# Kernel optimization log

Hardware: AMD Instinct MI355X
Metric: run time of the kernel (lower is better)

## Reference

```python
import jax, jax.numpy as jnp
from jax import lax
import numpy as np

G = 33            # LUT grid size per axis (hard-coded in module)
G3 = G * G * G    # 35937 entries per channel LUT


def _gelu(x):
    return jax.nn.gelu(x, approximate=False)  # torch nn.GELU default = exact erf


def _conv(x, w, b):
    # 3x3 stride-1 padding-1 conv == SAME padding, NCHW/OIHW like torch
    y = lax.conv_general_dilated(x, w, (1, 1), 'SAME',
                                 dimension_numbers=('NCHW', 'OIHW', 'NCHW'))
    return y + b[None, :, None, None]


def _bn(x, g, b, eps=1e-5):
    # eval-mode BatchNorm2d with running_mean=0, running_var=1
    s = g * (1.0 + eps) ** -0.5
    return x * s[None, :, None, None] + b[None, :, None, None]


def _resblock(x, wA, bA, gA, btA, wB, bB, gB, btB):
    h = _gelu(_bn(_conv(x, wA, bA), gA, btA))
    h = _bn(_conv(h, wB, bB), gB, btB)
    return _gelu(h + x)


def _apply_luts(luts_flat, recon):
    # Trilinear 3D-LUT sampling == F.grid_sample(mode='bilinear', padding_mode='border',
    # align_corners=True) on a 5D LUT. grid = recon[...,[2,1,0]]*2-1 means image ch0 (R)
    # indexes LUT dim 2, ch1 (G) dim 3, ch2 (B) dim 4; align_corners maps v->v*(G-1).
    # luts_flat: [B, L*3, G^3] (all num_luts fused into the channel dim, gathered once)
    # recon:     [B, 3, H, W] in [0,1]
    B, C3, _ = luts_flat.shape
    _, _, H, W = recon.shape
    c = jnp.clip(recon * (G - 1.0), 0.0, G - 1.0)      # border clamp
    f0 = jnp.clip(jnp.floor(c), 0.0, G - 2.0)
    t = c - f0                                          # fractional weights [B,3,H,W]
    i0 = f0.astype(jnp.int32)
    r0, g0, b0 = i0[:, 0], i0[:, 1], i0[:, 2]           # [B,H,W] each
    tr, tg, tb = t[:, 0], t[:, 1], t[:, 2]
    out = jnp.zeros((B, C3, H * W), dtype=luts_flat.dtype)
    for dr in (0, 1):
        for dg in (0, 1):
            for db in (0, 1):
                idx = ((r0 + dr) * G + (g0 + dg)) * G + (b0 + db)   # [B,H,W]
                w = ((tr if dr else 1.0 - tr) * (tg if dg else 1.0 - tg)
                     * (tb if db else 1.0 - tb))
                vals = jnp.take_along_axis(luts_flat, idx.reshape(B, 1, H * W), axis=2)
                out = out + vals * w.reshape(B, 1, H * W)
    return out.reshape(B, C3 // 3, 3, H, W)            # [B, L, 3, H, W]


def setup_inputs() -> dict:
    key = jax.random.key(0)
    ks = iter(jax.random.split(key, 32))
    def nrm(shape, s=0.02):
        return jax.random.normal(next(ks), shape, jnp.float32) * s
    B, T, V, E, HID, L, H, W = 4, 1024, 1024, 256, 256, 8, 384, 384
    inp = dict(
        tokens=jax.random.randint(next(ks), (B, T), 0, V),
        img=jax.random.uniform(next(ks), (B, 3, H, W), jnp.float32),
        recon_image=jax.random.uniform(next(ks), (B, 3, H, W), jnp.float32),
        emb_table=nrm((V, E)),
        agg_w1=nrm((E, HID)), agg_b1=jnp.zeros((HID,), jnp.float32),
        agg_w2=nrm((HID, HID)), agg_b2=jnp.zeros((HID,), jnp.float32),
        lut_w1=nrm((HID, HID)), lut_b1=jnp.zeros((HID,), jnp.float32),
        lut_w2=nrm((HID, L * 3 * G3), 0.005),
        lut_b2=jnp.zeros((L * 3 * G3,), jnp.float32),
        wg_w1=nrm((HID, HID // 4)), wg_b1=jnp.zeros((HID // 4,), jnp.float32),
        wg_w2=nrm((HID // 4, L)), wg_b2=jnp.zeros((L,), jnp.float32),
        rp_cin_w=nrm((32, 3, 3, 3)), rp_cin_b=jnp.zeros((32,), jnp.float32),
        rp_rbA_w=nrm((32, 32, 3, 3)), rp_rbA_b=jnp.zeros((32,), jnp.float32),
        rp_rbA_g=jnp.ones((32,), jnp.float32), rp_rbA_bt=jnp.zeros((32,), jnp.float32),
        rp_rbB_w=nrm((32, 32, 3, 3)), rp_rbB_b=jnp.zeros((32,), jnp.float32),
        rp_rbB_g=jnp.ones((32,), jnp.float32), rp_rbB_bt=jnp.zeros((32,), jnp.float32),
        rp_cout_w=nrm((3, 32, 3, 3)), rp_cout_b=jnp.zeros((3,), jnp.float32),
        fu_cin_w=nrm((32, 6, 3, 3)), fu_cin_b=jnp.zeros((32,), jnp.float32),
        fu_rbA_w=nrm((32, 32, 3, 3)), fu_rbA_b=jnp.zeros((32,), jnp.float32),
        fu_rbA_g=jnp.ones((32,), jnp.float32), fu_rbA_bt=jnp.zeros((32,), jnp.float32),
        fu_rbB_w=nrm((32, 32, 3, 3)), fu_rbB_b=jnp.zeros((32,), jnp.float32),
        fu_rbB_g=jnp.ones((32,), jnp.float32), fu_rbB_bt=jnp.zeros((32,), jnp.float32),
        fu_cout_w=nrm((3, 32, 3, 3)), fu_cout_b=jnp.zeros((3,), jnp.float32),
    )
    return inp


def reference(tokens, img, recon_image, emb_table,
              agg_w1, agg_b1, agg_w2, agg_b2,
              lut_w1, lut_b1, lut_w2, lut_b2,
              wg_w1, wg_b1, wg_w2, wg_b2,
              rp_cin_w, rp_cin_b, rp_rbA_w, rp_rbA_b, rp_rbA_g, rp_rbA_bt,
              rp_rbB_w, rp_rbB_b, rp_rbB_g, rp_rbB_bt, rp_cout_w, rp_cout_b,
              fu_cin_w, fu_cin_b, fu_rbA_w, fu_rbA_b, fu_rbA_g, fu_rbA_bt,
              fu_rbB_w, fu_rbB_b, fu_rbB_g, fu_rbB_bt, fu_cout_w, fu_cout_b):
    B = img.shape[0]
    L = wg_w2.shape[1]
    # token features
    emb = emb_table[tokens]                       # [B, T, E]
    tf = jnp.mean(emb, axis=1)                    # [B, E]
    tf = _gelu(tf @ agg_w1 + agg_b1) @ agg_w2 + agg_b2   # [B, HID]
    # dynamic LUTs and fusion weights
    lut_params = _gelu(tf @ lut_w1 + lut_b1) @ lut_w2 + lut_b2   # [B, L*3*G3]
    luts_flat = lut_params.reshape(B, L * 3, G3)
    lw = jax.nn.softmax(_gelu(tf @ wg_w1 + wg_b1) @ wg_w2 + wg_b2, axis=1)  # [B, L]
    # apply all LUTs in one fused gather pass, then weighted sum over LUTs
    lut_out = _apply_luts(luts_flat, recon_image)                # [B, L, 3, H, W]
    fused = jnp.einsum('blchw,bl->bchw', lut_out, lw)            # [B, 3, H, W]
    # residual processing branch on original img
    proc = _gelu(_conv(img, rp_cin_w, rp_cin_b))
    proc = _resblock(proc, rp_rbA_w, rp_rbA_b, rp_rbA_g, rp_rbA_bt,
                     rp_rbB_w, rp_rbB_b, rp_rbB_g, rp_rbB_bt)
    proc = _conv(proc, rp_cout_w, rp_cout_b)
    # fusion
    comb = jnp.concatenate([fused, proc], axis=1)                # [B, 6, H, W]
    out = _gelu(_conv(comb, fu_cin_w, fu_cin_b))
    out = _resblock(out, fu_rbA_w, fu_rbA_b, fu_rbA_g, fu_rbA_bt,
                    fu_rbB_w, fu_rbB_b, fu_rbB_g, fu_rbB_bt)
    out = _conv(out, fu_cout_w, fu_cout_b)
    return out + img
```

## Files before the change

kernel.cpp:

```cpp
#include <hip/hip_runtime.h>
#include <hip/hip_bf16.h>
#include <math.h>

#define BB    4
#define TT    1024
#define EE    256
#define HIDD  256
#define LLUT  8
#define HGT   384
#define WID   384
#define HWPX  147456
#define GSZ   33
#define G3    35937
#define NCOL  862488

typedef __attribute__((ext_vector_type(8))) short bf16x8;
typedef __attribute__((ext_vector_type(4))) float f32x4;

__device__ __forceinline__ float gelu_f(float x) {
    float s = 1.5957691216057308f * x * (1.0f + 0.044715f * x * x);
    float e = __expf(s);
    return x - x / (e + 1.0f);
}

__device__ __forceinline__ ushort f2bf(float x) {
    uint u = __float_as_uint(x);
    return (ushort)((u + 0x7FFFu + ((u >> 16) & 1u)) >> 16);
}
__device__ __forceinline__ uint pack2bf(float a, float b) {
    return (uint)f2bf(a) | ((uint)f2bf(b) << 16);
}
__device__ __forceinline__ float bf2f_lo(uint u) { return __uint_as_float(u << 16); }
__device__ __forceinline__ float bf2f_hi(uint u) { return __uint_as_float(u & 0xFFFF0000u); }

__global__ __launch_bounds__(256) void pack_wconv_kernel(
    const float* __restrict__ w0, const float* __restrict__ w1,
    const float* __restrict__ w2, const float* __restrict__ w3,
    ushort* __restrict__ wpk)
{
    const int layer = blockIdx.x;
    const float* w = (layer == 0) ? w0 : (layer == 1) ? w1 : (layer == 2) ? w2 : w3;
    ushort* dst = wpk + layer * 9216;
    for (int i = threadIdx.x; i < 9216; i += 256) {
        const int j    = i & 7;
        const int lane = (i >> 3) & 63;
        const int half = (i >> 9) & 1;
        const int tap  = i >> 10;
        const int co = half * 16 + (lane & 15);
        const int ci = (lane >> 4) * 8 + j;
        dst[i] = f2bf(w[co * 288 + ci * 9 + tap]);
    }
}

__global__ __launch_bounds__(256) void emb_partial_kernel(
    const int* __restrict__ tokens, const float* __restrict__ emb,
    float* __restrict__ partial)
{
    const int s = blockIdx.x, b = blockIdx.y, tid = threadIdx.x;
    const int* tok = tokens + b * TT + s * 16;
    float acc = 0.f;
#pragma unroll
    for (int t = 0; t < 16; ++t) acc += emb[tok[t] * EE + tid];
    partial[(b * 64 + s) * EE + tid] = acc;
}

__global__ __launch_bounds__(1024) void mlp_head_kernel(
    const float* __restrict__ partial,
    const float* __restrict__ aw1, const float* __restrict__ ab1,
    const float* __restrict__ aw2, const float* __restrict__ ab2,
    const float* __restrict__ lw1, const float* __restrict__ lb1,
    const float* __restrict__ gw1, const float* __restrict__ gb1,
    const float* __restrict__ gw2, const float* __restrict__ gb2,
    float* __restrict__ h3_out, float* __restrict__ lw_out)
{
    const int b = blockIdx.x;
    const int tid = threadIdx.x;
    const int o = tid & 255;
    const int q = tid >> 8;
    __shared__ float tf[256], h1[256], tf2s[256], h4[64], lg[8];
    __shared__ float red[4][256];

    {
        float acc = 0.f;
#pragma unroll
        for (int s = 0; s < 16; ++s)
            acc += partial[(b * 64 + q * 16 + s) * EE + o];
        red[q][o] = acc;
    }
    __syncthreads();
    if (tid < 256)
        tf[tid] = (red[0][tid] + red[1][tid] + red[2][tid] + red[3][tid]) * (1.0f / TT);
    __syncthreads();

    {
        float s = 0.f;
#pragma unroll 8
        for (int j = 0; j < 64; ++j) {
            const int k = (q << 6) + j;
            s += tf[k] * aw1[k * HIDD + o];
        }
        red[q][o] = s;
    }
    __syncthreads();
    if (tid < 256)
        h1[tid] = gelu_f(red[0][tid] + red[1][tid] + red[2][tid] + red[3][tid] + ab1[tid]);
    __syncthreads();

    {
        float s = 0.f;
#pragma unroll 8
        for (int j = 0; j < 64; ++j) {
            const int k = (q << 6) + j;
            s += h1[k] * aw2[k * HIDD + o];
        }
        red[q][o] = s;
    }
    __syncthreads();
    if (tid < 256)
        tf2s[tid] = red[0][tid] + red[1][tid] + red[2][tid] + red[3][tid] + ab2[tid];
    __syncthreads();

    {
        float s = 0.f;
#pragma unroll 8
        for (int j = 0; j < 64; ++j) {
            const int k = (q << 6) + j;
            s += tf2s[k] * lw1[k * HIDD + o];
        }
        red[q][o] = s;
    }
    __syncthreads();
    if (tid < 256)
        h3_out[b * HIDD + tid] =
            gelu_f(red[0][tid] + red[1][tid] + red[2][tid] + red[3][tid] + lb1[tid]);
    __syncthreads();

    {
        const int o64 = tid & 63, q16 = tid >> 6;
        float s = 0.f;
#pragma unroll
        for (int j = 0; j < 16; ++j) {
            const int k = q16 * 16 + j;
            s += tf2s[k] * gw1[k * 64 + o64];
        }
        ((float*)red)[q16 * 64 + o64] = s;
    }
    __syncthreads();
    if (tid < 64) {
        float s = gb1[tid];
#pragma unroll
        for (int r = 0; r < 16; ++r) s += ((float*)red)[r * 64 + tid];
        h4[tid] = gelu_f(s);
    }
    __syncthreads();

    if (tid < 8) {
        float s = gb2[tid];
#pragma unroll 8
        for (int k = 0; k < 64; ++k) s += h4[k] * gw2[k * LLUT + tid];
        lg[tid] = s;
    }
    __syncthreads();
    if (tid == 0) {
        float m = lg[0];
        for (int i = 1; i < LLUT; ++i) m = fmaxf(m, lg[i]);
        float ssum = 0.f, ex[LLUT];
        for (int i = 0; i < LLUT; ++i) { ex[i] = expf(lg[i] - m); ssum += ex[i]; }
        for (int i = 0; i < LLUT; ++i) lw_out[b * LLUT + i] = ex[i] / ssum;
    }
}

__global__ __launch_bounds__(256) void lut_fused_kernel(
    const float* __restrict__ h3, const float* __restrict__ lwv,
    const float* __restrict__ w2, const float* __restrict__ b2,
    float* __restrict__ clut)
{
    __shared__ float h[BB * HIDD];
    __shared__ float lws[BB * LLUT];
    const int tid = threadIdx.x;
    for (int i = tid; i < BB * HIDD; i += 256) h[i] = h3[i];
    if (tid < BB * LLUT) lws[tid] = lwv[tid];
    __syncthreads();

    const int idx = blockIdx.x * 256 + tid;
    if (idx >= 3 * G3) return;
    const int c = idx / G3, v = idx - c * G3;

    float acc[BB][LLUT];
#pragma unroll
    for (int b = 0; b < BB; ++b)
#pragma unroll
        for (int l = 0; l < LLUT; ++l) acc[b][l] = 0.f;

    const float* wbase = w2 + (long)c * G3 + v;
#pragma unroll 4
    for (int k = 0; k < HIDD; ++k) {
        const float* row = wbase + (long)k * NCOL;
        float wl[LLUT];
#pragma unroll
        for (int l = 0; l < LLUT; ++l) wl[l] = row[l * 3 * G3];
#pragma unroll
        for (int b = 0; b < BB; ++b) {
            const float hb = h[b * HIDD + k];
#pragma unroll
            for (int l = 0; l < LLUT; ++l) acc[b][l] += wl[l] * hb;
        }
    }

    float bb[LLUT];
#pragma unroll
    for (int l = 0; l < LLUT; ++l) bb[l] = b2[(long)(l * 3 + c) * G3 + v];

#pragma unroll
    for (int b = 0; b < BB; ++b) {
        float s = 0.f;
#pragma unroll
        for (int l = 0; l < LLUT; ++l) s += lws[b * LLUT + l] * (acc[b][l] + bb[l]);
        clut[(long)(b * 3 + c) * G3 + v] = s;
    }
}

__global__ __launch_bounds__(256) void applylut_out3_kernel(
    const float* __restrict__ clut, const float* __restrict__ recon,
    const ushort* __restrict__ act2, const float* __restrict__ wgt,
    const float* __restrict__ bias, ushort* __restrict__ comb)
{
    const int p = blockIdx.x * 256 + threadIdx.x;
    const int b = blockIdx.y;

    const float* rc = recon + (long)b * 3 * HWPX;
    float cr = fminf(fmaxf(rc[p] * 32.f, 0.f), 32.f);
    float cg = fminf(fmaxf(rc[HWPX + p] * 32.f, 0.f), 32.f);
    float cb = fminf(fmaxf(rc[2 * HWPX + p] * 32.f, 0.f), 32.f);
    float fr = fminf(floorf(cr), 31.f);
    float fg = fminf(floorf(cg), 31.f);
    float fb = fminf(floorf(cb), 31.f);
    float tr = cr - fr, tg = cg - fg, tb_ = cb - fb;
    int idx = (((int)fr * GSZ + (int)fg) * GSZ + (int)fb);
    float c[3];
#pragma unroll
    for (int ch = 0; ch < 3; ++ch) {
        const float* lut = clut + (long)(b * 3 + ch) * G3;
        float v000 = lut[idx],                  v001 = lut[idx + 1];
        float v010 = lut[idx + GSZ],            v011 = lut[idx + GSZ + 1];
        float v100 = lut[idx + GSZ * GSZ],      v101 = lut[idx + GSZ * GSZ + 1];
        float v110 = lut[idx + GSZ * GSZ + GSZ], v111 = lut[idx + GSZ * GSZ + GSZ + 1];
        float c00 = v000 + (v001 - v000) * tb_;
        float c01 = v010 + (v011 - v010) * tb_;
        float c10 = v100 + (v101 - v100) * tb_;
        float c11 = v110 + (v111 - v110) * tb_;
        float c0 = c00 + (c01 - c00) * tg;
        float c1 = c10 + (c11 - c10) * tg;
        c[ch] = c0 + (c1 - c0) * tr;
    }

    const int hh = p / WID, ww = p - hh * WID;
    float acc[3] = {bias[0], bias[1], bias[2]};
#pragma unroll
    for (int tap = 0; tap < 9; ++tap) {
        const int dh = tap / 3, dw = tap - dh * 3;
        const int gh = hh + dh - 1, gw = ww + dw - 1;
        if (gh < 0 || gh >= HGT || gw < 0 || gw >= WID) continue;
        const uint4* xp = (const uint4*)(act2 + ((long)b * HWPX + gh * WID + gw) * 32);
        float xx[32];
#pragma unroll
        for (int q = 0; q < 4; ++q) {
            uint4 v = xp[q];
            xx[q * 8 + 0] = bf2f_lo(v.x); xx[q * 8 + 1] = bf2f_hi(v.x);
            xx[q * 8 + 2] = bf2f_lo(v.y); xx[q * 8 + 3] = bf2f_hi(v.y);
            xx[q * 8 + 4] = bf2f_lo(v.z); xx[q * 8 + 5] = bf2f_hi(v.z);
            xx[q * 8 + 6] = bf2f_lo(v.w); xx[q * 8 + 7] = bf2f_hi(v.w);
        }
#pragma unroll
        for (int o = 0; o < 3; ++o)
#pragma unroll
            for (int ci = 0; ci < 32; ++ci)
                acc[o] += xx[ci] * wgt[o * 288 + ci * 9 + tap];
    }

    uint4 u;
    u.x = pack2bf(c[0], c[1]);
    u.y = pack2bf(c[2], 0.f);
    u.z = pack2bf(acc[0], acc[1]);
    u.w = pack2bf(acc[2], 0.f);
    *(uint4*)(comb + ((long)b * HWPX + p) * 8) = u;
}

__global__ __launch_bounds__(256) void conv_in3_kernel(
    const float* __restrict__ img, const float* __restrict__ wgt,
    const float* __restrict__ bias, ushort* __restrict__ out)
{
    const int tid = threadIdx.x;
    const int p0 = (blockIdx.x * 256 + tid) * 2;
    const int b = blockIdx.y;
    const int hh = p0 / WID, ww = p0 - hh * WID;

    float acc[32][2];
#pragma unroll
    for (int o = 0; o < 32; ++o) { float bv = bias[o]; acc[o][0] = bv; acc[o][1] = bv; }

    const bool wlo = (ww > 0), whi = (ww + 2 < WID);
#pragma unroll
    for (int ci = 0; ci < 3; ++ci) {
        const float* ip = img + (long)(b * 3 + ci) * HWPX;
        float x[3][4];
#pragma unroll
        for (int dh = 0; dh < 3; ++dh) {
            const int hs = hh + dh - 1;
            const bool hok = (hs >= 0) && (hs < HGT);
            const float* rp_ = ip + hs * WID + ww;
            x[dh][0] = (hok && wlo) ? rp_[-1] : 0.f;
            x[dh][1] = hok ? rp_[0] : 0.f;
            x[dh][2] = hok ? rp_[1] : 0.f;
            x[dh][3] = (hok && whi) ? rp_[2] : 0.f;
        }
#pragma unroll
        for (int o = 0; o < 32; ++o) {
            const float* wv = wgt + o * 27 + ci * 9;
#pragma unroll
            for (int dh = 0; dh < 3; ++dh)
#pragma unroll
                for (int dw = 0; dw < 3; ++dw) {
                    const float w = wv[dh * 3 + dw];
                    acc[o][0] += x[dh][dw]     * w;
                    acc[o][1] += x[dh][dw + 1] * w;
                }
        }
    }

    ushort* op = out + ((long)b * HWPX + p0) * 32;
#pragma unroll
    for (int px = 0; px < 2; ++px) {
        uint u[16];
#pragma unroll
        for (int o2 = 0; o2 < 16; ++o2)
            u[o2] = pack2bf(gelu_f(acc[2 * o2][px]), gelu_f(acc[2 * o2 + 1][px]));
        uint4* dst = (uint4*)(op + px * 32);
#pragma unroll
        for (int q = 0; q < 4; ++q)
            dst[q] = make_uint4(u[4 * q], u[4 * q + 1], u[4 * q + 2], u[4 * q + 3]);
    }
}

#define TH2 8
#define TW2 64
#define NTX (WID / TW2)
#define NTY (HGT / TH2)
#define NBLK (NTX * NTY * BB)
#define CHUNK (NBLK / 8)
#define HALO_H2 10
#define HALO_W2 66
#define CSTR 40

template <bool HAS_RES>
__global__ __launch_bounds__(512, 6) void conv32_mfma(
    const ushort* __restrict__ in, const ushort* __restrict__ res,
    const ushort* __restrict__ wpk, const float* __restrict__ bias,
    const float* __restrict__ bn_g, const float* __restrict__ bn_bt,
    ushort* __restrict__ out)
{
    __shared__ ushort halo[HALO_H2 * HALO_W2 * CSTR];
    __shared__ float s_scale[32], s_shift[32];

    const int tid = threadIdx.x;
    const int bid = blockIdx.x;
    const int t   = (bid & 7) * CHUNK + (bid >> 3);
    const int tx  = t % NTX;
    const int rem = t / NTX;
    const int ty  = rem % NTY;
    const int b   = rem / NTY;
    const int h0 = ty * TH2;
    const int w0 = tx * TW2;

    if (tid < 32) {
        float sg = bn_g[tid] * 0.9999950000375f;
        s_scale[tid] = sg;
        s_shift[tid] = bias[tid] * sg + bn_bt[tid];
    }

    const ushort* inb = in + (long)b * HWPX * 32;
    for (int i = tid; i < HALO_H2 * HALO_W2 * 4; i += 512) {
        const int row = i / (HALO_W2 * 4);
        const int rem2 = i - row * (HALO_W2 * 4);
        const int px = rem2 >> 2, q = rem2 & 3;
        const int gh = h0 + row - 1, gw = w0 + px - 1;
        uint4 v = make_uint4(0u, 0u, 0u, 0u);
        if (gh >= 0 && gh < HGT && gw >= 0 && gw < WID)
            v = *(const uint4*)(inb + ((long)gh * WID + gw) * 32 + q * 8);
        *(uint4*)(&halo[(row * HALO_W2 + px) * CSTR + q * 8]) = v;
    }
    __syncthreads();

    const int lane = tid & 63, wid = tid >> 6;
    const int l15 = lane & 15, kg = lane >> 4;
    const int r = wid;
    const ushort* wlane = wpk + lane * 8;

    f32x4 acc[4][2];
#pragma unroll
    for (int f = 0; f < 4; ++f)
#pragma unroll
        for (int cf = 0; cf < 2; ++cf)
            acc[f][cf] = (f32x4){0.f, 0.f, 0.f, 0.f};

#pragma unroll
    for (int tap = 0; tap < 9; ++tap) {
        const int dh = tap / 3, dw = tap - dh * 3;
        const bf16x8 a0 = *(const bf16x8*)(wlane + (tap * 2 + 0) * 512);
        const bf16x8 a1 = *(const bf16x8*)(wlane + (tap * 2 + 1) * 512);
#pragma unroll
        for (int f = 0; f < 4; ++f) {
            const int c0 = f * 16;
            const bf16x8 bfv = *(const bf16x8*)(
                &halo[((r + dh) * HALO_W2 + (c0 + dw + l15)) * CSTR + kg * 8]);
            acc[f][0] = __builtin_amdgcn_mfma_f32_16x16x32_bf16(a0, bfv, acc[f][0], 0, 0, 0);
            acc[f][1] = __builtin_amdgcn_mfma_f32_16x16x32_bf16(a1, bfv, acc[f][1], 0, 0, 0);
        }
    }

#pragma unroll
    for (int f = 0; f < 4; ++f) {
        const int c0 = f * 16;
        const long gpx = (long)b * HWPX + (long)(h0 + r) * WID + (w0 + c0 + l15);
#pragma unroll
        for (int cf = 0; cf < 2; ++cf) {
            const int co0 = cf * 16 + kg * 4;
            const float4 sc = *(const float4*)(&s_scale[co0]);
            const float4 sh = *(const float4*)(&s_shift[co0]);
            float v0 = acc[f][cf][0] * sc.x + sh.x;
            float v1 = acc[f][cf][1] * sc.y + sh.y;
            float v2 = acc[f][cf][2] * sc.z + sh.z;
            float v3 = acc[f][cf][3] * sc.w + sh.w;
            if (HAS_RES) {
                const uint2 rv = *(const uint2*)(res + gpx * 32 + co0);
                v0 += bf2f_lo(rv.x); v1 += bf2f_hi(rv.x);
                v2 += bf2f_lo(rv.y); v3 += bf2f_hi(rv.y);
            }
            uint2 o;
            o.x = pack2bf(gelu_f(v0), gelu_f(v1));
            o.y = pack2bf(gelu_f(v2), gelu_f(v3));
            *(uint2*)(out + gpx * 32 + co0) = o;
        }
    }
}

__global__ __launch_bounds__(256) void conv_in6_kernel(
    const ushort* __restrict__ comb, const float* __restrict__ wgt,
    const float* __restrict__ bias, ushort* __restrict__ out)
{
    const int p = blockIdx.x * 256 + threadIdx.x;
    const int b = blockIdx.y;
    const int hh = p / WID, ww = p - hh * WID;

    float acc[32];
#pragma unroll
    for (int o = 0; o < 32; ++o) acc[o] = bias[o];

#pragma unroll
    for (int tap = 0; tap < 9; ++tap) {
        const int dh = tap / 3, dw = tap - dh * 3;
        const int gh = hh + dh - 1, gw = ww + dw - 1;
        if (gh < 0 || gh >= HGT || gw < 0 || gw >= WID) continue;
        const uint4 v = *(const uint4*)(comb + ((long)b * HWPX + gh * WID + gw) * 8);
        const float xs[6] = {bf2f_lo(v.x), bf2f_hi(v.x), bf2f_lo(v.y),
                             bf2f_lo(v.z), bf2f_hi(v.z), bf2f_lo(v.w)};
#pragma unroll
        for (int o = 0; o < 32; ++o) {
            const float* wv = wgt + o * 54 + tap;
            acc[o] += xs[0] * wv[0]  + xs[1] * wv[9]  + xs[2] * wv[18]
                    + xs[3] * wv[27] + xs[4] * wv[36] + xs[5] * wv[45];
        }
    }

    ushort* op = out + ((long)b * HWPX + p) * 32;
    uint u[16];
#pragma unroll
    for (int o2 = 0; o2 < 16; ++o2)
        u[o2] = pack2bf(gelu_f(acc[2 * o2]), gelu_f(acc[2 * o2 + 1]));
    uint4* dst = (uint4*)op;
#pragma unroll
    for (int q = 0; q < 4; ++q)
        dst[q] = make_uint4(u[4 * q], u[4 * q + 1], u[4 * q + 2], u[4 * q + 3]);
}

__global__ __launch_bounds__(256) void conv_final_kernel(
    const ushort* __restrict__ in, const float* __restrict__ wgt,
    const float* __restrict__ bias, const float* __restrict__ img,
    float* __restrict__ outp)
{
    const int p = blockIdx.x * 256 + threadIdx.x;
    const int b = blockIdx.y;
    const int hh = p / WID, ww = p - hh * WID;
    float acc[3] = {bias[0], bias[1], bias[2]};

#pragma unroll
    for (int tap = 0; tap < 9; ++tap) {
        const int dh = tap / 3, dw = tap - dh * 3;
        const int gh = hh + dh - 1, gw = ww + dw - 1;
        if (gh < 0 || gh >= HGT || gw < 0 || gw >= WID) continue;
        const uint4* xp = (const uint4*)(in + ((long)b * HWPX + gh * WID + gw) * 32);
        float xx[32];
#pragma unroll
        for (int q = 0; q < 4; ++q) {
            uint4 v = xp[q];
            xx[q * 8 + 0] = bf2f_lo(v.x); xx[q * 8 + 1] = bf2f_hi(v.x);
            xx[q * 8 + 2] = bf2f_lo(v.y); xx[q * 8 + 3] = bf2f_hi(v.y);
            xx[q * 8 + 4] = bf2f_lo(v.z); xx[q * 8 + 5] = bf2f_hi(v.z);
            xx[q * 8 + 6] = bf2f_lo(v.w); xx[q * 8 + 7] = bf2f_hi(v.w);
        }
#pragma unroll
        for (int o = 0; o < 3; ++o)
#pragma unroll
            for (int ci = 0; ci < 32; ++ci)
                acc[o] += xx[ci] * wgt[o * 288 + ci * 9 + tap];
    }
#pragma unroll
    for (int o = 0; o < 3; ++o)
        outp[(long)(b * 3 + o) * HWPX + p] = acc[o] + img[(long)(b * 3 + o) * HWPX + p];
}

extern "C" void kernel_launch(void* const* d_in, const int* in_sizes, int n_in,
                              void* d_out, int out_size, void* d_ws, size_t ws_size,
                              hipStream_t stream)
{
    const int*   tokens  = (const int*)d_in[0];
    const float* img     = (const float*)d_in[1];
    const float* recon   = (const float*)d_in[2];
    const float* emb     = (const float*)d_in[3];
    const float* agg_w1  = (const float*)d_in[4];
    const float* agg_b1  = (const float*)d_in[5];
    const float* agg_w2  = (const float*)d_in[6];
    const float* agg_b2  = (const float*)d_in[7];
    const float* lut_w1  = (const float*)d_in[8];
    const float* lut_b1  = (const float*)d_in[9];
    const float* lut_w2  = (const float*)d_in[10];
    const float* lut_b2  = (const float*)d_in[11];
    const float* wg_w1   = (const float*)d_in[12];
    const float* wg_b1   = (const float*)d_in[13];
    const float* wg_w2   = (const float*)d_in[14];
    const float* wg_b2   = (const float*)d_in[15];
    const float* rp_cin_w = (const float*)d_in[16];
    const float* rp_cin_b = (const float*)d_in[17];
    const float* rp_rbA_w = (const float*)d_in[18];
    const float* rp_rbA_b = (const float*)d_in[19];
    const float* rp_rbA_g = (const float*)d_in[20];
    const float* rp_rbA_bt= (const float*)d_in[21];
    const float* rp_rbB_w = (const float*)d_in[22];
    const float* rp_rbB_b = (const float*)d_in[23];
    const float* rp_rbB_g = (const float*)d_in[24];
    const float* rp_rbB_bt= (const float*)d_in[25];
    const float* rp_cout_w= (const float*)d_in[26];
    const float* rp_cout_b= (const float*)d_in[27];
    const float* fu_cin_w = (const float*)d_in[28];
    const float* fu_cin_b = (const float*)d_in[29];
    const float* fu_rbA_w = (const float*)d_in[30];
    const float* fu_rbA_b = (const float*)d_in[31];
    const float* fu_rbA_g = (const float*)d_in[32];
    const float* fu_rbA_bt= (const float*)d_in[33];
    const float* fu_rbB_w = (const float*)d_in[34];
    const float* fu_rbB_b = (const float*)d_in[35];
    const float* fu_rbB_g = (const float*)d_in[36];
    const float* fu_rbB_bt= (const float*)d_in[37];
    const float* fu_cout_w= (const float*)d_in[38];
    const float* fu_cout_b= (const float*)d_in[39];

    float* ws = (float*)d_ws;
    float*  h3      = ws;
    float*  lwv     = ws + 1024;
    float*  partial = ws + 2048;
    float*  clut    = ws + 69632;
    ushort* wpack   = (ushort*)(ws + 524288);
    ushort* comb    = (ushort*)(ws + 589824);
    ushort* act0    = (ushort*)(ws + 3145728);
    ushort* act1    = (ushort*)(ws + 12582912);
    ushort* act2    = (ushort*)(ws + 22020096);
    float*  outp    = (float*)d_out;

    pack_wconv_kernel<<<dim3(4), dim3(256), 0, stream>>>(
        rp_rbA_w, rp_rbB_w, fu_rbA_w, fu_rbB_w, wpack);

    emb_partial_kernel<<<dim3(64, BB), dim3(256), 0, stream>>>(tokens, emb, partial);
    mlp_head_kernel<<<dim3(BB), dim3(1024), 0, stream>>>(
        partial, agg_w1, agg_b1, agg_w2, agg_b2,
        lut_w1, lut_b1, wg_w1, wg_b1, wg_w2, wg_b2, h3, lwv);

    lut_fused_kernel<<<dim3((3 * G3 + 255) / 256), dim3(256), 0, stream>>>(
        h3, lwv, lut_w2, lut_b2, clut);

    const dim3 g1(HWPX / 256, BB), g2(HWPX / 512, BB), blk(256);
    const dim3 gm(NBLK), bm(512);

    conv_in3_kernel<<<g2, blk, 0, stream>>>(img, rp_cin_w, rp_cin_b, act0);
    conv32_mfma<false><<<gm, bm, 0, stream>>>(
        act0, nullptr, wpack + 0 * 9216, rp_rbA_b, rp_rbA_g, rp_rbA_bt, act1);
    conv32_mfma<true><<<gm, bm, 0, stream>>>(
        act1, act0, wpack + 1 * 9216, rp_rbB_b, rp_rbB_g, rp_rbB_bt, act2);

    applylut_out3_kernel<<<g1, blk, 0, stream>>>(
        clut, recon, act2, rp_cout_w, rp_cout_b, comb);

    conv_in6_kernel<<<g1, blk, 0, stream>>>(comb, fu_cin_w, fu_cin_b, act0);
    conv32_mfma<false><<<gm, bm, 0, stream>>>(
        act0, nullptr, wpack + 2 * 9216, fu_rbA_b, fu_rbA_g, fu_rbA_bt, act1);
    conv32_mfma<true><<<gm, bm, 0, stream>>>(
        act1, act0, wpack + 3 * 9216, fu_rbB_b, fu_rbB_g, fu_rbB_bt, act2);
    conv_final_kernel<<<g1, blk, 0, stream>>>(act2, fu_cout_w, fu_cout_b, img, outp);
}
```

Measured before the change: 553.0 us.

## Split LUT generation across the first three residual-branch conv launches

```diff
diff --git a/kernel.cpp b/kernel.cpp
--- a/kernel.cpp
+++ b/kernel.cpp
@@ -13,6 +13,7 @@
 #define GSZ   33
 #define G3    35937
 #define NCOL  862488
+#define NOUT3 107811
 
 typedef __attribute__((ext_vector_type(8))) short bf16x8;
 typedef __attribute__((ext_vector_type(4))) float f32x4;
@@ -32,6 +33,49 @@
 }
 __device__ __forceinline__ float bf2f_lo(uint u) { return __uint_as_float(u << 16); }
 __device__ __forceinline__ float bf2f_hi(uint u) { return __uint_as_float(u & 0xFFFF0000u); }
+
+__device__ __forceinline__ void lut_one(
+    int idx, const float* __restrict__ hbuf,
+    const float* __restrict__ w2, const float* __restrict__ b2,
+    float* __restrict__ clut)
+{
+    if (idx >= NOUT3) return;
+    const int c = idx / G3, v = idx - c * G3;
+    const float* lws = hbuf + BB * HIDD;
+
+    float acc[BB][LLUT];
+#pragma unroll
+    for (int b = 0; b < BB; ++b)
+#pragma unroll
+        for (int l = 0; l < LLUT; ++l) acc[b][l] = 0.f;
+
+    const float* wbase = w2 + (long)c * G3 + v;
+#pragma unroll 4
+    for (int k = 0; k < HIDD; ++k) {
+        const float* row = wbase + (long)k * NCOL;
+        float wl[LLUT];
+#pragma unroll
+        for (int l = 0; l < LLUT; ++l) wl[l] = row[l * 3 * G3];
+#pragma unroll
+        for (int b = 0; b < BB; ++b) {
+            const float hb = hbuf[b * HIDD + k];
+#pragma unroll
+            for (int l = 0; l < LLUT; ++l) acc[b][l] += wl[l] * hb;
+        }
+    }
+
+    float bb[LLUT];
+#pragma unroll
+    for (int l = 0; l < LLUT; ++l) bb[l] = b2[(long)(l * 3 + c) * G3 + v];
+
+#pragma unroll
+    for (int b = 0; b < BB; ++b) {
+        float s = 0.f;
+#pragma unroll
+        for (int l = 0; l < LLUT; ++l) s += lws[b * LLUT + l] * (acc[b][l] + bb[l]);
+        clut[(long)(b * 3 + c) * G3 + v] = s;
+    }
+}
 
 __global__ __launch_bounds__(256) void pack_wconv_kernel(
     const float* __restrict__ w0, const float* __restrict__ w1,
@@ -170,129 +214,31 @@
     }
 }
 
-__global__ __launch_bounds__(256) void lut_fused_kernel(
+#define IN3_NB   1152
+#define LUT1_NB  108
+#define LUT1_CNT 27648
+
+__global__ __launch_bounds__(256) void conv_in3_lut_kernel(
+    const float* __restrict__ img, const float* __restrict__ wgt,
+    const float* __restrict__ bias, ushort* __restrict__ out,
     const float* __restrict__ h3, const float* __restrict__ lwv,
     const float* __restrict__ w2, const float* __restrict__ b2,
     float* __restrict__ clut)
 {
-    __shared__ float h[BB * HIDD];
-    __shared__ float lws[BB * LLUT];
+    __shared__ float hbuf[BB * HIDD + BB * LLUT];
     const int tid = threadIdx.x;
-    for (int i = tid; i < BB * HIDD; i += 256) h[i] = h3[i];
-    if (tid < BB * LLUT) lws[tid] = lwv[tid];
-    __syncthreads();
-
-    const int idx = blockIdx.x * 256 + tid;
-    if (idx >= 3 * G3) return;
-    const int c = idx / G3, v = idx - c * G3;
-
-    float acc[BB][LLUT];
-#pragma unroll
-    for (int b = 0; b < BB; ++b)
-#pragma unroll
-        for (int l = 0; l < LLUT; ++l) acc[b][l] = 0.f;
-
-    const float* wbase = w2 + (long)c * G3 + v;
-#pragma unroll 4
-    for (int k = 0; k < HIDD; ++k) {
-        const float* row = wbase + (long)k * NCOL;
-        float wl[LLUT];
-#pragma unroll
-        for (int l = 0; l < LLUT; ++l) wl[l] = row[l * 3 * G3];
-#pragma unroll
-        for (int b = 0; b < BB; ++b) {
-            const float hb = h[b * HIDD + k];
-#pragma unroll
-            for (int l = 0; l < LLUT; ++l) acc[b][l] += wl[l] * hb;
-        }
-    }
-
-    float bb[LLUT];
-#pragma unroll
-    for (int l = 0; l < LLUT; ++l) bb[l] = b2[(long)(l * 3 + c) * G3 + v];
-
-#pragma unroll
-    for (int b = 0; b < BB; ++b) {
-        float s = 0.f;
-#pragma unroll
-        for (int l = 0; l < LLUT; ++l) s += lws[b * LLUT + l] * (acc[b][l] + bb[l]);
-        clut[(long)(b * 3 + c) * G3 + v] = s;
-    }
-}
-
-__global__ __launch_bounds__(256) void applylut_out3_kernel(
-    const float* __restrict__ clut, const float* __restrict__ recon,
-    const ushort* __restrict__ act2, const float* __restrict__ wgt,
-    const float* __restrict__ bias, ushort* __restrict__ comb)
-{
-    const int p = blockIdx.x * 256 + threadIdx.x;
-    const int b = blockIdx.y;
-
-    const float* rc = recon + (long)b * 3 * HWPX;
-    float cr = fminf(fmaxf(rc[p] * 32.f, 0.f), 32.f);
-    float cg = fminf(fmaxf(rc[HWPX + p] * 32.f, 0.f), 32.f);
-    float cb = fminf(fmaxf(rc[2 * HWPX + p] * 32.f, 0.f), 32.f);
-    float fr = fminf(floorf(cr), 31.f);
-    float fg = fminf(floorf(cg), 31.f);
-    float fb = fminf(floorf(cb), 31.f);
-    float tr = cr - fr, tg = cg - fg, tb_ = cb - fb;
-    int idx = (((int)fr * GSZ + (int)fg) * GSZ + (int)fb);
-    float c[3];
-#pragma unroll
-    for (int ch = 0; ch < 3; ++ch) {
-        const float* lut = clut + (long)(b * 3 + ch) * G3;
-        float v000 = lut[idx],                  v001 = lut[idx + 1];
-        float v010 = lut[idx + GSZ],            v011 = lut[idx + GSZ + 1];
-        float v100 = lut[idx + GSZ * GSZ],      v101 = lut[idx + GSZ * GSZ + 1];
-        float v110 = lut[idx + GSZ * GSZ + GSZ], v111 = lut[idx + GSZ * GSZ + GSZ + 1];
-        float c00 = v000 + (v001 - v000) * tb_;
-        float c01 = v010 + (v011 - v010) * tb_;
-        float c10 = v100 + (v101 - v100) * tb_;
-        float c11 = v110 + (v111 - v110) * tb_;
-        float c0 = c00 + (c01 - c00) * tg;
-        float c1 = c10 + (c11 - c10) * tg;
-        c[ch] = c0 + (c1 - c0) * tr;
-    }
-
-    const int hh = p / WID, ww = p - hh * WID;
-    float acc[3] = {bias[0], bias[1], bias[2]};
-#pragma unroll
-    for (int tap = 0; tap < 9; ++tap) {
-        const int dh = tap / 3, dw = tap - dh * 3;
-        const int gh = hh + dh - 1, gw = ww + dw - 1;
-        if (gh < 0 || gh >= HGT || gw < 0 || gw >= WID) continue;
-        const uint4* xp = (const uint4*)(act2 + ((long)b * HWPX + gh * WID + gw) * 32);
-        float xx[32];
-#pragma unroll
-        for (int q = 0; q < 4; ++q) {
-            uint4 v = xp[q];
-            xx[q * 8 + 0] = bf2f_lo(v.x); xx[q * 8 + 1] = bf2f_hi(v.x);
-            xx[q * 8 + 2] = bf2f_lo(v.y); xx[q * 8 + 3] = bf2f_hi(v.y);
-            xx[q * 8 + 4] = bf2f_lo(v.z); xx[q * 8 + 5] = bf2f_hi(v.z);
-            xx[q * 8 + 6] = bf2f_lo(v.w); xx[q * 8 + 7] = bf2f_hi(v.w);
-        }
-#pragma unroll
-        for (int o = 0; o < 3; ++o)
-#pragma unroll
-            for (int ci = 0; ci < 32; ++ci)
-                acc[o] += xx[ci] * wgt[o * 288 + ci * 9 + tap];
-    }
-
-    uint4 u;
-    u.x = pack2bf(c[0], c[1]);
-    u.y = pack2bf(c[2], 0.f);
-    u.z = pack2bf(acc[0], acc[1]);
-    u.w = pack2bf(acc[2], 0.f);
-    *(uint4*)(comb + ((long)b * HWPX + p) * 8) = u;
-}
-
-__global__ __launch_bounds__(256) void conv_in3_kernel(
-    const float* __restrict__ img, const float* __restrict__ wgt,
-    const float* __restrict__ bias, ushort* __restrict__ out)
-{
-    const int tid = threadIdx.x;
-    const int p0 = (blockIdx.x * 256 + tid) * 2;
-    const int b = blockIdx.y;
+    const int bid = blockIdx.x;
+
+    if (bid >= IN3_NB) {
+        for (int i = tid; i < BB * HIDD; i += 256) hbuf[i] = h3[i];
+        if (tid < BB * LLUT) hbuf[BB * HIDD + tid] = lwv[tid];
+        __syncthreads();
+        lut_one((bid - IN3_NB) * 256 + tid, hbuf, w2, b2, clut);
+        return;
+    }
+
+    const int b = bid / 288, xb = bid - b * 288;
+    const int p0 = (xb * 256 + tid) * 2;
     const int hh = p0 / WID, ww = p0 - hh * WID;
 
     float acc[32][2];
@@ -357,13 +303,26 @@
     const ushort* __restrict__ in, const ushort* __restrict__ res,
     const ushort* __restrict__ wpk, const float* __restrict__ bias,
     const float* __restrict__ bn_g, const float* __restrict__ bn_bt,
-    ushort* __restrict__ out)
+    ushort* __restrict__ out,
+    const float* __restrict__ h3, const float* __restrict__ lwv,
+    const float* __restrict__ w2, const float* __restrict__ b2,
+    float* __restrict__ clut, int lut_off)
 {
     __shared__ ushort halo[HALO_H2 * HALO_W2 * CSTR];
     __shared__ float s_scale[32], s_shift[32];
 
     const int tid = threadIdx.x;
     const int bid = blockIdx.x;
+
+    if (bid >= NBLK) {
+        float* hbuf = (float*)halo;
+        for (int i = tid; i < BB * HIDD; i += 512) hbuf[i] = h3[i];
+        if (tid < BB * LLUT) hbuf[BB * HIDD + tid] = lwv[tid];
+        __syncthreads();
+        lut_one((bid - NBLK) * 512 + tid + lut_off, hbuf, w2, b2, clut);
+        return;
+    }
+
     const int t   = (bid & 7) * CHUNK + (bid >> 3);
     const int tx  = t % NTX;
     const int rem = t / NTX;
@@ -442,6 +401,72 @@
             *(uint2*)(out + gpx * 32 + co0) = o;
         }
     }
+}
+
+__global__ __launch_bounds__(256) void applylut_out3_kernel(
+    const float* __restrict__ clut, const float* __restrict__ recon,
+    const ushort* __restrict__ act2, const float* __restrict__ wgt,
+    const float* __restrict__ bias, ushort* __restrict__ comb)
+{
+    const int p = blockIdx.x * 256 + threadIdx.x;
+    const int b = blockIdx.y;
+
+    const float* rc = recon + (long)b * 3 * HWPX;
+    float cr = fminf(fmaxf(rc[p] * 32.f, 0.f), 32.f);
+    float cg = fminf(fmaxf(rc[HWPX + p] * 32.f, 0.f), 32.f);
+    float cb = fminf(fmaxf(rc[2 * HWPX + p] * 32.f, 0.f), 32.f);
+    float fr = fminf(floorf(cr), 31.f);
+    float fg = fminf(floorf(cg), 31.f);
+    float fb = fminf(floorf(cb), 31.f);
+    float tr = cr - fr, tg = cg - fg, tb_ = cb - fb;
+    int idx = (((int)fr * GSZ + (int)fg) * GSZ + (int)fb);
+    float c[3];
+#pragma unroll
+    for (int ch = 0; ch < 3; ++ch) {
+        const float* lut = clut + (long)(b * 3 + ch) * G3;
+        float v000 = lut[idx],                  v001 = lut[idx + 1];
+        float v010 = lut[idx + GSZ],            v011 = lut[idx + GSZ + 1];
+        float v100 = lut[idx + GSZ * GSZ],      v101 = lut[idx + GSZ * GSZ + 1];
+        float v110 = lut[idx + GSZ * GSZ + GSZ], v111 = lut[idx + GSZ * GSZ + GSZ + 1];
+        float c00 = v000 + (v001 - v000) * tb_;
+        float c01 = v010 + (v011 - v010) * tb_;
+        float c10 = v100 + (v101 - v100) * tb_;
+        float c11 = v110 + (v111 - v110) * tb_;
+        float c0 = c00 + (c01 - c00) * tg;
+        float c1 = c10 + (c11 - c10) * tg;
+        c[ch] = c0 + (c1 - c0) * tr;
+    }
+
+    const int hh = p / WID, ww = p - hh * WID;
+    float acc[3] = {bias[0], bias[1], bias[2]};
+#pragma unroll
+    for (int tap = 0; tap < 9; ++tap) {
+        const int dh = tap / 3, dw = tap - dh * 3;
+        const int gh = hh + dh - 1, gw = ww + dw - 1;
+        if (gh < 0 || gh >= HGT || gw < 0 || gw >= WID) continue;
+        const uint4* xp = (const uint4*)(act2 + ((long)b * HWPX + gh * WID + gw) * 32);
+        float xx[32];
+#pragma unroll
+        for (int q = 0; q < 4; ++q) {
+            uint4 v = xp[q];
+            xx[q * 8 + 0] = bf2f_lo(v.x); xx[q * 8 + 1] = bf2f_hi(v.x);
+            xx[q * 8 + 2] = bf2f_lo(v.y); xx[q * 8 + 3] = bf2f_hi(v.y);
+            xx[q * 8 + 4] = bf2f_lo(v.z); xx[q * 8 + 5] = bf2f_hi(v.z);
+            xx[q * 8 + 6] = bf2f_lo(v.w); xx[q * 8 + 7] = bf2f_hi(v.w);
+        }
+#pragma unroll
+        for (int o = 0; o < 3; ++o)
+#pragma unroll
+            for (int ci = 0; ci < 32; ++ci)
+                acc[o] += xx[ci] * wgt[o * 288 + ci * 9 + tap];
+    }
+
+    uint4 u;
+    u.x = pack2bf(c[0], c[1]);
+    u.y = pack2bf(c[2], 0.f);
+    u.z = pack2bf(acc[0], acc[1]);
+    u.w = pack2bf(acc[2], 0.f);
+    *(uint4*)(comb + ((long)b * HWPX + p) * 8) = u;
 }
 
 __global__ __launch_bounds__(256) void conv_in6_kernel(
@@ -576,6 +601,10 @@
     ushort* act2    = (ushort*)(ws + 22020096);
     float*  outp    = (float*)d_out;
 
+    const int LUT2_NB = 79;
+    const int LUT3_NB = 78;
+    const int OFF2 = 27648, OFF3 = 68096;
+
     pack_wconv_kernel<<<dim3(4), dim3(256), 0, stream>>>(
         rp_rbA_w, rp_rbB_w, fu_rbA_w, fu_rbB_w, wpack);
 
@@ -584,25 +613,26 @@
         partial, agg_w1, agg_b1, agg_w2, agg_b2,
         lut_w1, lut_b1, wg_w1, wg_b1, wg_w2, wg_b2, h3, lwv);
 
-    lut_fused_kernel<<<dim3((3 * G3 + 255) / 256), dim3(256), 0, stream>>>(
-        h3, lwv, lut_w2, lut_b2, clut);
-
-    const dim3 g1(HWPX / 256, BB), g2(HWPX / 512, BB), blk(256);
-    const dim3 gm(NBLK), bm(512);
-
-    conv_in3_kernel<<<g2, blk, 0, stream>>>(img, rp_cin_w, rp_cin_b, act0);
-    conv32_mfma<false><<<gm, bm, 0, stream>>>(
-        act0, nullptr, wpack + 0 * 9216, rp_rbA_b, rp_rbA_g, rp_rbA_bt, act1);
-    conv32_mfma<true><<<gm, bm, 0, stream>>>(
-        act1, act0, wpack + 1 * 9216, rp_rbB_b, rp_rbB_g, rp_rbB_bt, act2);
+    const dim3 g1(HWPX / 256, BB), blk(256);
+
+    conv_in3_lut_kernel<<<dim3(IN3_NB + LUT1_NB), blk, 0, stream>>>(
+        img, rp_cin_w, rp_cin_b, act0, h3, lwv, lut_w2, lut_b2, clut);
+    conv32_mfma<false><<<dim3(NBLK + LUT2_NB), dim3(512), 0, stream>>>(
+        act0, nullptr, wpack + 0 * 9216, rp_rbA_b, rp_rbA_g, rp_rbA_bt, act1,
+        h3, lwv, lut_w2, lut_b2, clut, OFF2);
+    conv32_mfma<true><<<dim3(NBLK + LUT3_NB), dim3(512), 0, stream>>>(
+        act1, act0, wpack + 1 * 9216, rp_rbB_b, rp_rbB_g, rp_rbB_bt, act2,
+        h3, lwv, lut_w2, lut_b2, clut, OFF3);
 
     applylut_out3_kernel<<<g1, blk, 0, stream>>>(
         clut, recon, act2, rp_cout_w, rp_cout_b, comb);
 
     conv_in6_kernel<<<g1, blk, 0, stream>>>(comb, fu_cin_w, fu_cin_b, act0);
-    conv32_mfma<false><<<gm, bm, 0, stream>>>(
-        act0, nullptr, wpack + 2 * 9216, fu_rbA_b, fu_rbA_g, fu_rbA_bt, act1);
-    conv32_mfma<true><<<gm, bm, 0, stream>>>(
-        act1, act0, wpack + 3 * 9216, fu_rbB_b, fu_rbB_g, fu_rbB_bt, act2);
+    conv32_mfma<false><<<dim3(NBLK), dim3(512), 0, stream>>>(
+        act0, nullptr, wpack + 2 * 9216, fu_rbA_b, fu_rbA_g, fu_rbA_bt, act1,
+        h3, lwv, lut_w2, lut_b2, clut, 0);
+    conv32_mfma<true><<<dim3(NBLK), dim3(512), 0, stream>>>(
+        act1, act0, wpack + 3 * 9216, fu_rbB_b, fu_rbB_g, fu_rbB_bt, act2,
+        h3, lwv, lut_w2, lut_b2, clut, 0);
     conv_final_kernel<<<g1, blk, 0, stream>>>(act2, fu_cout_w, fu_cout_b, img, outp);
 }
```

Result: slower. 990.6 us (+79.1%).

## Move 32->3 and 6->32 convs onto MFMA with LDS halo tiles

Applied to the files above, without the earlier changes.

```diff
diff --git a/kernel.cpp b/kernel.cpp
--- a/kernel.cpp
+++ b/kernel.cpp
@@ -33,22 +33,54 @@
 __device__ __forceinline__ float bf2f_lo(uint u) { return __uint_as_float(u << 16); }
 __device__ __forceinline__ float bf2f_hi(uint u) { return __uint_as_float(u & 0xFFFF0000u); }
 
+#define TH2 8
+#define TW2 64
+#define NTX (WID / TW2)
+#define NTY (HGT / TH2)
+#define NBLK (NTX * NTY * BB)
+#define CHUNK (NBLK / 8)
+#define HALO_H2 10
+#define HALO_W2 66
+#define CSTR 40
+
 __global__ __launch_bounds__(256) void pack_wconv_kernel(
     const float* __restrict__ w0, const float* __restrict__ w1,
     const float* __restrict__ w2, const float* __restrict__ w3,
-    ushort* __restrict__ wpk)
+    const float* __restrict__ c0w, const float* __restrict__ c1w,
+    const float* __restrict__ w6, ushort* __restrict__ wpk)
 {
     const int layer = blockIdx.x;
-    const float* w = (layer == 0) ? w0 : (layer == 1) ? w1 : (layer == 2) ? w2 : w3;
-    ushort* dst = wpk + layer * 9216;
-    for (int i = threadIdx.x; i < 9216; i += 256) {
-        const int j    = i & 7;
-        const int lane = (i >> 3) & 63;
-        const int half = (i >> 9) & 1;
-        const int tap  = i >> 10;
-        const int co = half * 16 + (lane & 15);
-        const int ci = (lane >> 4) * 8 + j;
-        dst[i] = f2bf(w[co * 288 + ci * 9 + tap]);
+    if (layer < 6) {
+        const float* w = (layer == 0) ? w0 : (layer == 1) ? w1 :
+                         (layer == 2) ? w2 : (layer == 3) ? w3 :
+                         (layer == 4) ? c0w : c1w;
+        const bool small = (layer >= 4);
+        ushort* dst = wpk + layer * 9216;
+        for (int i = threadIdx.x; i < 9216; i += 256) {
+            const int j    = i & 7;
+            const int lane = (i >> 3) & 63;
+            const int half = (i >> 9) & 1;
+            const int tap  = i >> 10;
+            const int co = half * 16 + (lane & 15);
+            const int ci = (lane >> 4) * 8 + j;
+            float v = 0.f;
+            if (!small || co < 3) v = w[co * 288 + ci * 9 + tap];
+            dst[i] = f2bf(v);
+        }
+    } else {
+        ushort* dst = wpk + 6 * 9216;
+        for (int i = threadIdx.x; i < 2048; i += 256) {
+            const int j    = i & 7;
+            const int lane = (i >> 3) & 63;
+            const int half = (i >> 9) & 1;
+            const int ks   = i >> 10;
+            const int co = half * 16 + (lane & 15);
+            const int k  = ks * 32 + (lane >> 4) * 8 + j;
+            float v = 0.f;
+            if (k < 54) { const int tap = k / 6, ci = k - 6 * tap;
+                          v = w6[co * 54 + ci * 9 + tap]; }
+            dst[i] = f2bf(v);
+        }
     }
 }
 
@@ -220,10 +252,9 @@
     }
 }
 
-__global__ __launch_bounds__(256) void applylut_out3_kernel(
+__global__ __launch_bounds__(256) void applylut_kernel(
     const float* __restrict__ clut, const float* __restrict__ recon,
-    const ushort* __restrict__ act2, const float* __restrict__ wgt,
-    const float* __restrict__ bias, ushort* __restrict__ comb)
+    ushort* __restrict__ comb)
 {
     const int p = blockIdx.x * 256 + threadIdx.x;
     const int b = blockIdx.y;
@@ -253,37 +284,10 @@
         float c1 = c10 + (c11 - c10) * tg;
         c[ch] = c0 + (c1 - c0) * tr;
     }
-
-    const int hh = p / WID, ww = p - hh * WID;
-    float acc[3] = {bias[0], bias[1], bias[2]};
-#pragma unroll
-    for (int tap = 0; tap < 9; ++tap) {
-        const int dh = tap / 3, dw = tap - dh * 3;
-        const int gh = hh + dh - 1, gw = ww + dw - 1;
-        if (gh < 0 || gh >= HGT || gw < 0 || gw >= WID) continue;
-        const uint4* xp = (const uint4*)(act2 + ((long)b * HWPX + gh * WID + gw) * 32);
-        float xx[32];
-#pragma unroll
-        for (int q = 0; q < 4; ++q) {
-            uint4 v = xp[q];
-            xx[q * 8 + 0] = bf2f_lo(v.x); xx[q * 8 + 1] = bf2f_hi(v.x);
-            xx[q * 8 + 2] = bf2f_lo(v.y); xx[q * 8 + 3] = bf2f_hi(v.y);
-            xx[q * 8 + 4] = bf2f_lo(v.z); xx[q * 8 + 5] = bf2f_hi(v.z);
-            xx[q * 8 + 6] = bf2f_lo(v.w); xx[q * 8 + 7] = bf2f_hi(v.w);
-        }
-#pragma unroll
-        for (int o = 0; o < 3; ++o)
-#pragma unroll
-            for (int ci = 0; ci < 32; ++ci)
-                acc[o] += xx[ci] * wgt[o * 288 + ci * 9 + tap];
-    }
-
-    uint4 u;
+    uint2 u;
     u.x = pack2bf(c[0], c[1]);
     u.y = pack2bf(c[2], 0.f);
-    u.z = pack2bf(acc[0], acc[1]);
-    u.w = pack2bf(acc[2], 0.f);
-    *(uint4*)(comb + ((long)b * HWPX + p) * 8) = u;
+    *(uint2*)(comb + ((long)b * HWPX + p) * 8) = u;
 }
 
 __global__ __launch_bounds__(256) void conv_in3_kernel(
@@ -341,16 +345,6 @@
             dst[q] = make_uint4(u[4 * q], u[4 * q + 1], u[4 * q + 2], u[4 * q + 3]);
     }
 }
-
-#define TH2 8
-#define TW2 64
-#define NTX (WID / TW2)
-#define NTY (HGT / TH2)
-#define NBLK (NTX * NTY * BB)
-#define CHUNK (NBLK / 8)
-#define HALO_H2 10
-#define HALO_W2 66
-#define CSTR 40
 
 template <bool HAS_RES>
 __global__ __launch_bounds__(512, 6) void conv32_mfma(
@@ -444,79 +438,167 @@
     }
 }
 
-__global__ __launch_bounds__(256) void conv_in6_kernel(
-    const ushort* __restrict__ comb, const float* __restrict__ wgt,
-    const float* __restrict__ bias, ushort* __restrict__ out)
-{
-    const int p = blockIdx.x * 256 + threadIdx.x;
-    const int b = blockIdx.y;
-    const int hh = p / WID, ww = p - hh * WID;
-
-    float acc[32];
-#pragma unroll
-    for (int o = 0; o < 32; ++o) acc[o] = bias[o];
+template <bool FINAL>
+__global__ __launch_bounds__(512, 4) void conv_out3_mfma(
+    const ushort* __restrict__ in, const ushort* __restrict__ wpk,
+    const float* __restrict__ bias, const float* __restrict__ img,
+    float* __restrict__ outp, ushort* __restrict__ comb)
+{
+    __shared__ ushort halo[HALO_H2 * HALO_W2 * CSTR];
+
+    const int tid = threadIdx.x;
+    const int bid = blockIdx.x;
+    const int t   = (bid & 7) * CHUNK + (bid >> 3);
+    const int tx  = t % NTX;
+    const int rem = t / NTX;
+    const int ty  = rem % NTY;
+    const int b   = rem / NTY;
+    const int h0 = ty * TH2;
+    const int w0 = tx * TW2;
+
+    const ushort* inb = in + (long)b * HWPX * 32;
+    for (int i = tid; i < HALO_H2 * HALO_W2 * 4; i += 512) {
+        const int row = i / (HALO_W2 * 4);
+        const int rem2 = i - row * (HALO_W2 * 4);
+        const int px = rem2 >> 2, q = rem2 & 3;
+        const int gh = h0 + row - 1, gw = w0 + px - 1;
+        uint4 v = make_uint4(0u, 0u, 0u, 0u);
+        if (gh >= 0 && gh < HGT && gw >= 0 && gw < WID)
+            v = *(const uint4*)(inb + ((long)gh * WID + gw) * 32 + q * 8);
+        *(uint4*)(&halo[(row * HALO_W2 + px) * CSTR + q * 8]) = v;
+    }
+    __syncthreads();
+
+    const int lane = tid & 63, wid = tid >> 6;
+    const int l15 = lane & 15, kg = lane >> 4;
+    const int r = wid;
+    const ushort* wlane = wpk + lane * 8;
+
+    f32x4 acc[4];
+#pragma unroll
+    for (int f = 0; f < 4; ++f) acc[f] = (f32x4){0.f, 0.f, 0.f, 0.f};
 
 #pragma unroll
     for (int tap = 0; tap < 9; ++tap) {
         const int dh = tap / 3, dw = tap - dh * 3;
-        const int gh = hh + dh - 1, gw = ww + dw - 1;
-        if (gh < 0 || gh >= HGT || gw < 0 || gw >= WID) continue;
-        const uint4 v = *(const uint4*)(comb + ((long)b * HWPX + gh * WID + gw) * 8);
-        const float xs[6] = {bf2f_lo(v.x), bf2f_hi(v.x), bf2f_lo(v.y),
-                             bf2f_lo(v.z), bf2f_hi(v.z), bf2f_lo(v.w)};
-#pragma unroll
-        for (int o = 0; o < 32; ++o) {
-            const float* wv = wgt + o * 54 + tap;
-            acc[o] += xs[0] * wv[0]  + xs[1] * wv[9]  + xs[2] * wv[18]
-                    + xs[3] * wv[27] + xs[4] * wv[36] + xs[5] * wv[45];
-        }
-    }
-
-    ushort* op = out + ((long)b * HWPX + p) * 32;
-    uint u[16];
-#pragma unroll
-    for (int o2 = 0; o2 < 16; ++o2)
-        u[o2] = pack2bf(gelu_f(acc[2 * o2]), gelu_f(acc[2 * o2 + 1]));
-    uint4* dst = (uint4*)op;
-#pragma unroll
-    for (int q = 0; q < 4; ++q)
-        dst[q] = make_uint4(u[4 * q], u[4 * q + 1], u[4 * q + 2], u[4 * q + 3]);
-}
-
-__global__ __launch_bounds__(256) void conv_final_kernel(
-    const ushort* __restrict__ in, const float* __restrict__ wgt,
-    const float* __restrict__ bias, const float* __restrict__ img,
-    float* __restrict__ outp)
-{
-    const int p = blockIdx.x * 256 + threadIdx.x;
-    const int b = blockIdx.y;
-    const int hh = p / WID, ww = p - hh * WID;
-    float acc[3] = {bias[0], bias[1], bias[2]};
-
-#pragma unroll
-    for (int tap = 0; tap < 9; ++tap) {
-        const int dh = tap / 3, dw = tap - dh * 3;
-        const int gh = hh + dh - 1, gw = ww + dw - 1;
-        if (gh < 0 || gh >= HGT || gw < 0 || gw >= WID) continue;
-        const uint4* xp = (const uint4*)(in + ((long)b * HWPX + gh * WID + gw) * 32);
-        float xx[32];
-#pragma unroll
-        for (int q = 0; q < 4; ++q) {
-            uint4 v = xp[q];
-            xx[q * 8 + 0] = bf2f_lo(v.x); xx[q * 8 + 1] = bf2f_hi(v.x);
-            xx[q * 8 + 2] = bf2f_lo(v.y); xx[q * 8 + 3] = bf2f_hi(v.y);
-            xx[q * 8 + 4] = bf2f_lo(v.z); xx[q * 8 + 5] = bf2f_hi(v.z);
-            xx[q * 8 + 6] = bf2f_lo(v.w); xx[q * 8 + 7] = bf2f_hi(v.w);
-        }
-#pragma unroll
-        for (int o = 0; o < 3; ++o)
-#pragma unroll
-            for (int ci = 0; ci < 32; ++ci)
-                acc[o] += xx[ci] * wgt[o * 288 + ci * 9 + tap];
-    }
-#pragma unroll
-    for (int o = 0; o < 3; ++o)
-        outp[(long)(b * 3 + o) * HWPX + p] = acc[o] + img[(long)(b * 3 + o) * HWPX + p];
+        const bf16x8 a0 = *(const bf16x8*)(wlane + (tap * 2 + 0) * 512);
+#pragma unroll
+        for (int f = 0; f < 4; ++f) {
+            const int c0 = f * 16;
+            const bf16x8 bfv = *(const bf16x8*)(
+                &halo[((r + dh) * HALO_W2 + (c0 + dw + l15)) * CSTR + kg * 8]);
+            acc[f] = __builtin_amdgcn_mfma_f32_16x16x32_bf16(a0, bfv, acc[f], 0, 0, 0);
+        }
+    }
+
+    if (kg == 0) {
+        const float b0 = bias[0], b1 = bias[1], b2v = bias[2];
+#pragma unroll
+        for (int f = 0; f < 4; ++f) {
+            const int p = (h0 + r) * WID + (w0 + f * 16 + l15);
+            const long gpx = (long)b * HWPX + p;
+            float v0 = acc[f][0] + b0;
+            float v1 = acc[f][1] + b1;
+            float v2 = acc[f][2] + b2v;
+            if (FINAL) {
+                outp[(long)(b * 3 + 0) * HWPX + p] = v0 + img[(long)(b * 3 + 0) * HWPX + p];
+                outp[(long)(b * 3 + 1) * HWPX + p] = v1 + img[(long)(b * 3 + 1) * HWPX + p];
+                outp[(long)(b * 3 + 2) * HWPX + p] = v2 + img[(long)(b * 3 + 2) * HWPX + p];
+            } else {
+                uint2 u;
+                u.x = pack2bf(v0, v1);
+                u.y = pack2bf(v2, 0.f);
+                *(uint2*)(comb + gpx * 8 + 4) = u;
+            }
+        }
+    }
+}
+
+__global__ __launch_bounds__(512) void conv_in6_mfma(
+    const ushort* __restrict__ comb, const ushort* __restrict__ wpk6,
+    const float* __restrict__ bias, ushort* __restrict__ out)
+{
+    __shared__ ushort chalo[HALO_H2 * HALO_W2 * 8];
+    __shared__ float s_bias[32];
+
+    const int tid = threadIdx.x;
+    const int bid = blockIdx.x;
+    const int t   = (bid & 7) * CHUNK + (bid >> 3);
+    const int tx  = t % NTX;
+    const int rem = t / NTX;
+    const int ty  = rem % NTY;
+    const int b   = rem / NTY;
+    const int h0 = ty * TH2;
+    const int w0 = tx * TW2;
+
+    if (tid < 32) s_bias[tid] = bias[tid];
+
+    const ushort* cb = comb + (long)b * HWPX * 8;
+    for (int i = tid; i < HALO_H2 * HALO_W2; i += 512) {
+        const int row = i / HALO_W2, px = i - row * HALO_W2;
+        const int gh = h0 + row - 1, gw = w0 + px - 1;
+        uint4 v = make_uint4(0u, 0u, 0u, 0u);
+        if (gh >= 0 && gh < HGT && gw >= 0 && gw < WID)
+            v = *(const uint4*)(cb + ((long)gh * WID + gw) * 8);
+        *(uint4*)(&chalo[i * 8]) = v;
+    }
+    __syncthreads();
+
+    const int lane = tid & 63, wid = tid >> 6;
+    const int l15 = lane & 15, kg = lane >> 4;
+    const int r = wid;
+    const ushort* wl6 = wpk6 + lane * 8;
+
+    f32x4 acc[4][2];
+#pragma unroll
+    for (int f = 0; f < 4; ++f)
+#pragma unroll
+        for (int cf = 0; cf < 2; ++cf)
+            acc[f][cf] = (f32x4){0.f, 0.f, 0.f, 0.f};
+
+#pragma unroll
+    for (int ks = 0; ks < 2; ++ks) {
+        const bf16x8 a0 = *(const bf16x8*)(wl6 + (ks * 2 + 0) * 512);
+        const bf16x8 a1 = *(const bf16x8*)(wl6 + (ks * 2 + 1) * 512);
+#pragma unroll
+        for (int f = 0; f < 4; ++f) {
+            const int c0 = f * 16;
+            bf16x8 bv;
+#pragma unroll
+            for (int j = 0; j < 8; ++j) {
+                const int k = ks * 32 + kg * 8 + j;
+                ushort val = 0;
+                if (k < 54) {
+                    const int tap = k / 6, ci = k - 6 * tap;
+                    const int dh = tap / 3, dwp = tap - 3 * dh;
+                    const int slot = ci + (ci >= 3 ? 1 : 0);
+                    val = chalo[((r + dh) * HALO_W2 + (c0 + dwp + l15)) * 8 + slot];
+                }
+                bv[j] = (short)val;
+            }
+            acc[f][0] = __builtin_amdgcn_mfma_f32_16x16x32_bf16(a0, bv, acc[f][0], 0, 0, 0);
+            acc[f][1] = __builtin_amdgcn_mfma_f32_16x16x32_bf16(a1, bv, acc[f][1], 0, 0, 0);
+        }
+    }
+
+#pragma unroll
+    for (int f = 0; f < 4; ++f) {
+        const int c0 = f * 16;
+        const long gpx = (long)b * HWPX + (long)(h0 + r) * WID + (w0 + c0 + l15);
+#pragma unroll
+        for (int cf = 0; cf < 2; ++cf) {
+            const int co0 = cf * 16 + kg * 4;
+            const float4 bv4 = *(const float4*)(&s_bias[co0]);
+            float v0 = acc[f][cf][0] + bv4.x;
+            float v1 = acc[f][cf][1] + bv4.y;
+            float v2 = acc[f][cf][2] + bv4.z;
+            float v3 = acc[f][cf][3] + bv4.w;
+            uint2 o;
+            o.x = pack2bf(gelu_f(v0), gelu_f(v1));
+            o.y = pack2bf(gelu_f(v2), gelu_f(v3));
+            *(uint2*)(out + gpx * 32 + co0) = o;
+        }
+    }
 }
 
 extern "C" void kernel_launch(void* const* d_in, const int* in_sizes, int n_in,
@@ -576,8 +658,9 @@
     ushort* act2    = (ushort*)(ws + 22020096);
     float*  outp    = (float*)d_out;
 
-    pack_wconv_kernel<<<dim3(4), dim3(256), 0, stream>>>(
-        rp_rbA_w, rp_rbB_w, fu_rbA_w, fu_rbB_w, wpack);
+    pack_wconv_kernel<<<dim3(7), dim3(256), 0, stream>>>(
+        rp_rbA_w, rp_rbB_w, fu_rbA_w, fu_rbB_w, rp_cout_w, fu_cout_w,
+        fu_cin_w, wpack);
 
     emb_partial_kernel<<<dim3(64, BB), dim3(256), 0, stream>>>(tokens, emb, partial);
     mlp_head_kernel<<<dim3(BB), dim3(1024), 0, stream>>>(
@@ -596,13 +679,15 @@
     conv32_mfma<true><<<gm, bm, 0, stream>>>(
         act1, act0, wpack + 1 * 9216, rp_rbB_b, rp_rbB_g, rp_rbB_bt, act2);
 
-    applylut_out3_kernel<<<g1, blk, 0, stream>>>(
-        clut, recon, act2, rp_cout_w, rp_cout_b, comb);
-
-    conv_in6_kernel<<<g1, blk, 0, stream>>>(comb, fu_cin_w, fu_cin_b, act0);
+    applylut_kernel<<<g1, blk, 0, stream>>>(clut, recon, comb);
+    conv_out3_mfma<false><<<gm, bm, 0, stream>>>(
+        act2, wpack + 4 * 9216, rp_cout_b, nullptr, nullptr, comb);
+
+    conv_in6_mfma<<<gm, bm, 0, stream>>>(comb, wpack + 6 * 9216, fu_cin_b, act0);
     conv32_mfma<false><<<gm, bm, 0, stream>>>(
         act0, nullptr, wpack + 2 * 9216, fu_rbA_b, fu_rbA_g, fu_rbA_bt, act1);
     conv32_mfma<true><<<gm, bm, 0, stream>>>(
         act1, act0, wpack + 3 * 9216, fu_rbB_b, fu_rbB_g, fu_rbB_bt, act2);
-    conv_final_kernel<<<g1, blk, 0, stream>>>(act2, fu_cout_w, fu_cout_b, img, outp);
-}
+    conv_out3_mfma<true><<<gm, bm, 0, stream>>>(
+        act2, wpack + 5 * 9216, fu_cout_b, img, outp, nullptr);
+}
```

Result: faster. 508.4 us (-8.1%).
